# Kernel optimization log

Hardware: AMD Instinct MI355X
Metric: run time of the kernel (lower is better)

The kernel has to match this reference:

```python
import jax, jax.numpy as jnp
import numpy as np

C = 4096
C8 = C // 8  # 512, must equal h*w
B, H, W = 32, 16, 32


def setup_inputs() -> dict:
    key = jax.random.key(0)
    ks = jax.random.split(key, 8)
    s = 0.02
    return {
        "x": jax.random.normal(ks[0], (B, C, H, W), dtype=jnp.float32),
        "Wq": jax.random.normal(ks[1], (C8, C), dtype=jnp.float32) * s,
        "bq": jax.random.normal(ks[2], (C8,), dtype=jnp.float32) * s,
        "Wk": jax.random.normal(ks[3], (C8, C), dtype=jnp.float32) * s,
        "bk": jax.random.normal(ks[4], (C8,), dtype=jnp.float32) * s,
        "Wv": jax.random.normal(ks[5], (C, C), dtype=jnp.float32) * s,
        "bv": jax.random.normal(ks[6], (C,), dtype=jnp.float32) * s,
        "gamma": jax.random.normal(ks[7], (1,), dtype=jnp.float32),
    }


def reference(x, Wq, bq, Wk, bk, Wv, bv, gamma):
    b, c, h, w = x.shape
    xf = x.reshape(b, c, h * w)               # (b, c, hw)
    # 1x1 conv == per-position linear over channels
    q = jnp.einsum("oc,bcl->bol", Wq, xf) + bq[None, :, None]   # (b, c8, hw)
    k = jnp.einsum("oc,bcl->bol", Wk, xf) + bk[None, :, None]   # (b, c8, hw)
    v = jnp.einsum("oc,bcl->bol", Wv, xf) + bv[None, :, None]   # (b, c, hw)
    # energy = bmm(Q, K^T): (b, c8, c8); no sqrt(d) scaling (faithful)
    energy = jnp.einsum("bol,bpl->bop", q, k)
    attn = jax.nn.softmax(energy, axis=-1)
    # out = bmm(V, attn^T): out[b,c,p] = sum_k V[b,c,k] * attn[b,p,k]
    out = jnp.einsum("bck,bpk->bcp", v, attn)  # requires hw == c8
    out = out.reshape(b, c, h, w)
    return gamma * out + x
```

## Files before the change

### kernel.cpp

```cpp
#include <hip/hip_runtime.h>


typedef _Float16 f16;
typedef _Float16 h8 __attribute__((ext_vector_type(8)));
typedef _Float16 h4 __attribute__((ext_vector_type(4)));
typedef float fx4 __attribute__((ext_vector_type(4)));

#define CC  4096
#define C8  512
#define HWD 512
#define NB  32

__device__ __forceinline__ void stage_tile(const f16* __restrict__ g, f16* __restrict__ s, int ld) {
  const int t = threadIdx.x;
#pragma unroll
  for (int i = 0; i < 4; ++i) {
    const int id = t + i * 256;
    const int r = id >> 3, j = id & 7;
    const uint4 v = *reinterpret_cast<const uint4*>(g + (long)r * ld + (j << 3));
    char* p = reinterpret_cast<char*>(s);
    const int b = ((r << 7) + (j << 4)) ^ ((r & 7) << 4);
    *reinterpret_cast<uint4*>(p + b) = v;
  }
}

__device__ __forceinline__ h8 ldfrag(const f16* s, int row, int kb) {
  const int b = ((row << 7) + kb) ^ ((row & 7) << 4);
  return *reinterpret_cast<const h8*>(reinterpret_cast<const char*>(s) + b);
}

template<bool TRIPLE, int EPI>
__global__ __launch_bounds__(256) void gemm_ker(
    const f16* __restrict__ Ah, const f16* __restrict__ Al,
    const f16* __restrict__ Bh, const f16* __restrict__ Bl,
    int K, int lda, int ldb, long sAb, long sBb, long sCb, int ldc,
    const float* __restrict__ bias,
    float* __restrict__ Cf, f16* __restrict__ Ch, f16* __restrict__ Cl,
    const float* __restrict__ resid, const float* __restrict__ gam)
{
  constexpr int TILE = 128 * 64;
  __shared__ __align__(16) f16 smem[(TRIPLE ? 4 : 2) * TILE];
  f16* sAh = smem;
  f16* sBh = smem + TILE;
  f16* sAl = TRIPLE ? smem + 2 * TILE : nullptr;
  f16* sBl = TRIPLE ? smem + 3 * TILE : nullptr;

  const int bz = blockIdx.z;
  const int m0 = blockIdx.y * 128, n0 = blockIdx.x * 128;
  const f16* gA = Ah + (long)bz * sAb + (long)m0 * lda;
  const f16* gB = Bh + (long)bz * sBb + (long)n0 * ldb;

  const int lane = threadIdx.x & 63;
  const int wid  = threadIdx.x >> 6;
  const int wr = wid >> 1, wc = wid & 1;
  const int frow = lane & 15;
  const int kq = (lane >> 4) << 4;

  fx4 acc[4][4] = {};

  for (int k0 = 0; k0 < K; k0 += 64) {
    stage_tile(gA + k0, sAh, lda);
    stage_tile(gB + k0, sBh, ldb);
    if constexpr (TRIPLE) {
      stage_tile(Al + (long)bz * sAb + (long)m0 * lda + k0, sAl, lda);
      stage_tile(Bl + (long)bz * sBb + (long)n0 * ldb + k0, sBl, ldb);
    }
    __syncthreads();
#pragma unroll
    for (int ks = 0; ks < 2; ++ks) {
      const int kb = ks * 64 + kq;
      h8 aH[4], bH[4];
      h8 aL[4], bL[4];
#pragma unroll
      for (int f = 0; f < 4; ++f) {
        aH[f] = ldfrag(sAh, wr * 64 + f * 16 + frow, kb);
        bH[f] = ldfrag(sBh, wc * 64 + f * 16 + frow, kb);
        if constexpr (TRIPLE) {
          aL[f] = ldfrag(sAl, wr * 64 + f * 16 + frow, kb);
          bL[f] = ldfrag(sBl, wc * 64 + f * 16 + frow, kb);
        }
      }
#pragma unroll
      for (int fm = 0; fm < 4; ++fm)
#pragma unroll
        for (int fn = 0; fn < 4; ++fn) {
          acc[fm][fn] = __builtin_amdgcn_mfma_f32_16x16x32_f16(aH[fm], bH[fn], acc[fm][fn], 0, 0, 0);
          if constexpr (TRIPLE) {
            acc[fm][fn] = __builtin_amdgcn_mfma_f32_16x16x32_f16(aH[fm], bL[fn], acc[fm][fn], 0, 0, 0);
            acc[fm][fn] = __builtin_amdgcn_mfma_f32_16x16x32_f16(aL[fm], bH[fn], acc[fm][fn], 0, 0, 0);
          }
        }
    }
    __syncthreads();
  }

  const int cm = (lane >> 4) * 4;
  const int cn = lane & 15;
  const float g0 = (EPI == 3) ? gam[0] : 0.f;
#pragma unroll
  for (int fm = 0; fm < 4; ++fm) {
    const int gr0 = m0 + wr * 64 + fm * 16 + cm;
#pragma unroll
    for (int fn = 0; fn < 4; ++fn) {
      const int gc = n0 + wc * 64 + fn * 16 + cn;
#pragma unroll
      for (int j = 0; j < 4; ++j) {
        const int gr = gr0 + j;
        const long ci = (long)bz * sCb + (long)gr * ldc + gc;
        float v = acc[fm][fn][j];
        if constexpr (EPI == 0) {
          v += bias[gr];
          const f16 h = (f16)v;
          Ch[ci] = h;
          Cl[ci] = (f16)(v - (float)h);
        } else if constexpr (EPI == 1) {
          Ch[ci] = (f16)(v + bias[gr]);
        } else if constexpr (EPI == 2) {
          Cf[ci] = v;
        } else {
          Cf[ci] = g0 * v + resid[ci];
        }
      }
    }
  }
}

__global__ void transpose_split_k(const float* __restrict__ x, f16* __restrict__ xh, f16* __restrict__ xl) {
  __shared__ float t[32][33];
  const int l0 = blockIdx.x * 32, c0 = blockIdx.y * 32;
  const long bi = (long)blockIdx.z * CC * HWD;
  const long bo = (long)blockIdx.z * HWD * CC;
  const int tx = threadIdx.x, ty = threadIdx.y;
#pragma unroll
  for (int i = 0; i < 32; i += 8)
    t[ty + i][tx] = x[bi + (long)(c0 + ty + i) * HWD + l0 + tx];
  __syncthreads();
#pragma unroll
  for (int i = 0; i < 32; i += 8) {
    const float v = t[tx][ty + i];
    const f16 h = (f16)v;
    const long o = bo + (long)(l0 + ty + i) * CC + c0 + tx;
    xh[o] = h;
    xl[o] = (f16)(v - (float)h);
  }
}

template<bool HASLO>
__global__ void split_k(const float* __restrict__ in, f16* __restrict__ hi, f16* __restrict__ lo, long n) {
  const long i = ((long)blockIdx.x * blockDim.x + threadIdx.x) * 4;
  if (i >= n) return;
  const float4 v = *reinterpret_cast<const float4*>(in + i);
  const float vv[4] = {v.x, v.y, v.z, v.w};
  h4 h, l;
#pragma unroll
  for (int j = 0; j < 4; ++j) {
    const f16 hh = (f16)vv[j];
    h[j] = hh;
    l[j] = (f16)(vv[j] - (float)hh);
  }
  *reinterpret_cast<h4*>(hi + i) = h;
  if constexpr (HASLO) *reinterpret_cast<h4*>(lo + i) = l;
}

__global__ __launch_bounds__(256) void softmax_k(const float* __restrict__ E, f16* __restrict__ attn) {
  const int lane = threadIdx.x & 63;
  const int wid  = threadIdx.x >> 6;
  const long row = (long)blockIdx.x * 4 + wid;
  const float* e = E + row * 512;
  const float4 a = *reinterpret_cast<const float4*>(e + lane * 8);
  const float4 b = *reinterpret_cast<const float4*>(e + lane * 8 + 4);
  float vv[8] = {a.x, a.y, a.z, a.w, b.x, b.y, b.z, b.w};
  float m = vv[0];
#pragma unroll
  for (int i = 1; i < 8; ++i) m = fmaxf(m, vv[i]);
#pragma unroll
  for (int s = 32; s > 0; s >>= 1) m = fmaxf(m, __shfl_xor(m, s));
  float sum = 0.f;
  float ex[8];
#pragma unroll
  for (int i = 0; i < 8; ++i) { ex[i] = __expf(vv[i] - m); sum += ex[i]; }
#pragma unroll
  for (int s = 32; s > 0; s >>= 1) sum += __shfl_xor(sum, s);
  const float inv = 1.f / sum;
  h8 o;
#pragma unroll
  for (int i = 0; i < 8; ++i) o[i] = (f16)(ex[i] * inv);
  *reinterpret_cast<h8*>(attn + row * 512 + lane * 8) = o;
}

extern "C" void kernel_launch(void* const* d_in, const int* in_sizes, int n_in,
                              void* d_out, int out_size, void* d_ws, size_t ws_size,
                              hipStream_t stream) {
  const float* x  = (const float*)d_in[0];
  const float* Wq = (const float*)d_in[1];
  const float* bq = (const float*)d_in[2];
  const float* Wk = (const float*)d_in[3];
  const float* bk = (const float*)d_in[4];
  const float* Wv = (const float*)d_in[5];
  const float* bv = (const float*)d_in[6];
  const float* gm = (const float*)d_in[7];
  float* out = (float*)d_out;

  const size_t szXT = (size_t)NB * HWD * CC;
  const size_t szQK = (size_t)NB * C8 * HWD;
  const size_t szW  = (size_t)C8 * CC;
  const size_t szWv = (size_t)CC * CC;
  const size_t needBytes = (2 * szXT + 4 * szQK + 4 * szW + szWv) * sizeof(f16);
  if (ws_size < needBytes) return;

  f16* xT_h = (f16*)d_ws;
  f16* xT_l = xT_h + szXT;
  f16* v16  = xT_l;
  f16* q_h  = xT_h + 2 * szXT;
  f16* q_l  = q_h + szQK;
  f16* k_h  = q_l + szQK;
  f16* k_l  = k_h + szQK;
  f16* wq_h = k_l + szQK;
  f16* wq_l = wq_h + szW;
  f16* wk_h = wq_l + szW;
  f16* wk_l = wk_h + szW;
  f16* attn = wq_h;
  f16* wv_h = wk_l + szW;
  float* E  = (float*)wv_h;

  split_k<true ><<<dim3((C8 * CC) / 1024), 256, 0, stream>>>(Wq, wq_h, wq_l, (long)C8 * CC);
  split_k<true ><<<dim3((C8 * CC) / 1024), 256, 0, stream>>>(Wk, wk_h, wk_l, (long)C8 * CC);
  split_k<false><<<dim3((CC * CC) / 1024), 256, 0, stream>>>(Wv, wv_h, nullptr, (long)CC * CC);
  transpose_split_k<<<dim3(HWD / 32, CC / 32, NB), dim3(32, 8), 0, stream>>>(x, xT_h, xT_l);
  gemm_ker<true, 0><<<dim3(4, 4, NB), 256, 0, stream>>>(wq_h, wq_l, xT_h, xT_l, CC, CC, CC,
      0L, (long)HWD * CC, (long)C8 * HWD, HWD, bq, nullptr, q_h, q_l, nullptr, nullptr);
  gemm_ker<true, 0><<<dim3(4, 4, NB), 256, 0, stream>>>(wk_h, wk_l, xT_h, xT_l, CC, CC, CC,
      0L, (long)HWD * CC, (long)C8 * HWD, HWD, bk, nullptr, k_h, k_l, nullptr, nullptr);
  gemm_ker<false, 1><<<dim3(4, 32, NB), 256, 0, stream>>>(wv_h, nullptr, xT_h, nullptr, CC, CC, CC,
      0L, (long)HWD * CC, (long)CC * HWD, HWD, bv, nullptr, v16, nullptr, nullptr, nullptr);
  gemm_ker<true, 2><<<dim3(4, 4, NB), 256, 0, stream>>>(q_h, q_l, k_h, k_l, HWD, HWD, HWD,
      (long)C8 * HWD, (long)C8 * HWD, (long)C8 * C8, C8, nullptr, E, nullptr, nullptr, nullptr, nullptr);
  softmax_k<<<dim3(NB * C8 / 4), 256, 0, stream>>>(E, attn);
  gemm_ker<false, 3><<<dim3(4, 32, NB), 256, 0, stream>>>(v16, nullptr, attn, nullptr, HWD, HWD, HWD,
      (long)CC * HWD, (long)C8 * HWD, (long)CC * HWD, HWD, nullptr, out, nullptr, nullptr, x, gm);
}
```

Measured before the change: 1.468 ms.

## Add double-buffered 256x256 GEMM with direct global-to-LDS loads for V and output

Adds a new GEMM kernel that uses 256x256 output tiles with 512 threads and double-buffered LDS filled by global_load_lds. It interleaves fragment loads with MFMA issue and raises wave priority during MFMA runs. The kernel also remaps blocks so consecutive workgroups share operand tiles. It replaces the two big single-precision-f16 GEMMs (V projection and attn-V output) to cut per-tile load/sync stalls and raise reuse. The old kernel is trimmed to a triple-f16 variant for the Q/K GEMMs. The large LDS footprint (128KB) and hand-placed waitcnts risk occupancy limits and correctness if the counts are wrong.

```diff
diff --git a/kernel.cpp b/kernel.cpp
--- a/kernel.cpp
+++ b/kernel.cpp
@@ -10,6 +10,117 @@
 #define C8  512
 #define HWD 512
 #define NB  32
+
+
+__device__ __forceinline__ h8 ldfragC(const char* s, int row, int cb) {
+  const int b = ((row << 7) | cb) ^ ((row & 7) << 4);
+  return *reinterpret_cast<const h8*>(s + b);
+}
+
+#define AS1C(p) ((const __attribute__((address_space(1))) unsigned int*)(p))
+#define AS3(p)  ((__attribute__((address_space(3))) unsigned int*)(p))
+
+#define STAGE(bufsel) { \
+  char* la_ = smem + ((bufsel) << 16); \
+  char* lb_ = la_ + 32768; \
+  _Pragma("unroll") for (int q = 0; q < 4; ++q) { \
+    __builtin_amdgcn_global_load_lds(AS1C(pA[q]), AS3(la_ + (q << 13) + w1024), 16, 0, 0); \
+    __builtin_amdgcn_global_load_lds(AS1C(pB[q]), AS3(lb_ + (q << 13) + w1024), 16, 0, 0); \
+    pA[q] += 128; pB[q] += 128; } }
+
+#define LOADA(hm) { \
+  _Pragma("unroll") for (int f = 0; f < 4; ++f) \
+  _Pragma("unroll") for (int ks = 0; ks < 2; ++ks) \
+    a[f][ks] = ldfragC(At, wr * 128 + (hm) * 64 + f * 16 + frow, ks * 64 + kq); }
+
+#define LOADB(hn) { \
+  _Pragma("unroll") for (int g = 0; g < 2; ++g) \
+  _Pragma("unroll") for (int ks = 0; ks < 2; ++ks) \
+    b[g][ks] = ldfragC(Bt, wc * 64 + (hn) * 32 + g * 16 + frow, ks * 64 + kq); }
+
+#define MMA(hm, hn) { \
+  __builtin_amdgcn_s_setprio(1); \
+  _Pragma("unroll") for (int f = 0; f < 4; ++f) \
+  _Pragma("unroll") for (int g = 0; g < 2; ++g) \
+  _Pragma("unroll") for (int ks = 0; ks < 2; ++ks) \
+    acc[(hm) * 4 + f][(hn) * 2 + g] = __builtin_amdgcn_mfma_f32_16x16x32_f16( \
+        a[f][ks], b[g][ks], acc[(hm) * 4 + f][(hn) * 2 + g], 0, 0, 0); \
+  __builtin_amdgcn_s_setprio(0); }
+
+template<int EPI>
+__global__ __launch_bounds__(512, 2) void gemm256(
+    const f16* __restrict__ Ah, const f16* __restrict__ Bh,
+    int lda, int ldb, long sAb, long sBb, long sCb, int ldc, int K,
+    const float* __restrict__ bias, float* __restrict__ Cf, f16* __restrict__ Ch,
+    const float* __restrict__ resid, const float* __restrict__ gam)
+{
+  extern __shared__ __align__(16) char smem[];
+  const int F  = blockIdx.x;
+  const int Vv = ((F & 7) << 7) | (F >> 3);
+  const int bz = Vv >> 5;
+  const int m0 = (Vv & 15) << 8;
+  const int n0 = ((Vv >> 4) & 1) << 8;
+
+  const int T = threadIdx.x;
+  const int lane = T & 63;
+  const int w = T >> 6;
+  const int wr = w >> 2, wc = w & 3;
+  const int frow = lane & 15;
+  const int kq = (lane >> 4) << 4;
+  const int w1024 = w << 10;
+
+  const int rr = T >> 3;
+  const int corig = ((T & 7) << 4) ^ ((rr & 7) << 4);
+  const char* pA[4];
+  const char* pB[4];
+#pragma unroll
+  for (int q = 0; q < 4; ++q) {
+    pA[q] = (const char*)(Ah + bz * sAb + (long)(m0 + q * 64 + rr) * lda) + corig;
+    pB[q] = (const char*)(Bh + bz * sBb + (long)(n0 + q * 64 + rr) * ldb) + corig;
+  }
+
+  fx4 acc[8][4] = {};
+  const int nt = K >> 6;
+
+  STAGE(0)
+  for (int t = 0; t < nt; ++t) {
+    if (t + 1 < nt) {
+      STAGE((t + 1) & 1)
+      asm volatile("s_waitcnt vmcnt(8)" ::: "memory");
+    } else {
+      asm volatile("s_waitcnt vmcnt(0)" ::: "memory");
+    }
+    asm volatile("s_barrier" ::: "memory");
+    const char* At = smem + ((t & 1) << 16);
+    const char* Bt = At + 32768;
+    h8 a[4][2], b[2][2];
+    LOADA(0) LOADB(0) MMA(0, 0)
+    LOADA(1)          MMA(1, 0)
+              LOADB(1) MMA(1, 1)
+    LOADA(0)          MMA(0, 1)
+    __builtin_amdgcn_sched_barrier(0);
+    asm volatile("s_waitcnt lgkmcnt(0)" ::: "memory");
+    asm volatile("s_barrier" ::: "memory");
+  }
+
+  const int cm = (lane >> 4) << 2;
+  const int cn = lane & 15;
+  const float g0 = (EPI == 3) ? gam[0] : 0.f;
+#pragma unroll
+  for (int fm = 0; fm < 8; ++fm) {
+    const int gr0 = m0 + wr * 128 + fm * 16 + cm;
+#pragma unroll
+    for (int fn = 0; fn < 4; ++fn) {
+      const int gc = n0 + wc * 64 + fn * 16 + cn;
+#pragma unroll
+      for (int j = 0; j < 4; ++j) {
+        const long ci = bz * sCb + (long)(gr0 + j) * ldc + gc;
+        if constexpr (EPI == 1) Ch[ci] = (f16)(acc[fm][fn][j] + bias[gr0 + j]);
+        else                    Cf[ci] = g0 * acc[fm][fn][j] + resid[ci];
+      }
+    }
+  }
+}
 
 __device__ __forceinline__ void stage_tile(const f16* __restrict__ g, f16* __restrict__ s, int ld) {
   const int t = threadIdx.x;
@@ -29,21 +140,20 @@
   return *reinterpret_cast<const h8*>(reinterpret_cast<const char*>(s) + b);
 }
 
-template<bool TRIPLE, int EPI>
-__global__ __launch_bounds__(256) void gemm_ker(
+template<int EPI>
+__global__ __launch_bounds__(256) void gemm_tri(
     const f16* __restrict__ Ah, const f16* __restrict__ Al,
     const f16* __restrict__ Bh, const f16* __restrict__ Bl,
     int K, int lda, int ldb, long sAb, long sBb, long sCb, int ldc,
     const float* __restrict__ bias,
-    float* __restrict__ Cf, f16* __restrict__ Ch, f16* __restrict__ Cl,
-    const float* __restrict__ resid, const float* __restrict__ gam)
+    float* __restrict__ Cf, f16* __restrict__ Ch, f16* __restrict__ Cl)
 {
   constexpr int TILE = 128 * 64;
-  __shared__ __align__(16) f16 smem[(TRIPLE ? 4 : 2) * TILE];
+  __shared__ __align__(16) f16 smem[4 * TILE];
   f16* sAh = smem;
   f16* sBh = smem + TILE;
-  f16* sAl = TRIPLE ? smem + 2 * TILE : nullptr;
-  f16* sBl = TRIPLE ? smem + 3 * TILE : nullptr;
+  f16* sAl = smem + 2 * TILE;
+  f16* sBl = smem + 3 * TILE;
 
   const int bz = blockIdx.z;
   const int m0 = blockIdx.y * 128, n0 = blockIdx.x * 128;
@@ -61,34 +171,27 @@
   for (int k0 = 0; k0 < K; k0 += 64) {
     stage_tile(gA + k0, sAh, lda);
     stage_tile(gB + k0, sBh, ldb);
-    if constexpr (TRIPLE) {
-      stage_tile(Al + (long)bz * sAb + (long)m0 * lda + k0, sAl, lda);
-      stage_tile(Bl + (long)bz * sBb + (long)n0 * ldb + k0, sBl, ldb);
-    }
+    stage_tile(Al + (long)bz * sAb + (long)m0 * lda + k0, sAl, lda);
+    stage_tile(Bl + (long)bz * sBb + (long)n0 * ldb + k0, sBl, ldb);
     __syncthreads();
 #pragma unroll
     for (int ks = 0; ks < 2; ++ks) {
       const int kb = ks * 64 + kq;
-      h8 aH[4], bH[4];
-      h8 aL[4], bL[4];
+      h8 aH[4], bH[4], aL[4], bL[4];
 #pragma unroll
       for (int f = 0; f < 4; ++f) {
         aH[f] = ldfrag(sAh, wr * 64 + f * 16 + frow, kb);
         bH[f] = ldfrag(sBh, wc * 64 + f * 16 + frow, kb);
-        if constexpr (TRIPLE) {
-          aL[f] = ldfrag(sAl, wr * 64 + f * 16 + frow, kb);
-          bL[f] = ldfrag(sBl, wc * 64 + f * 16 + frow, kb);
-        }
+        aL[f] = ldfrag(sAl, wr * 64 + f * 16 + frow, kb);
+        bL[f] = ldfrag(sBl, wc * 64 + f * 16 + frow, kb);
       }
 #pragma unroll
       for (int fm = 0; fm < 4; ++fm)
 #pragma unroll
         for (int fn = 0; fn < 4; ++fn) {
           acc[fm][fn] = __builtin_amdgcn_mfma_f32_16x16x32_f16(aH[fm], bH[fn], acc[fm][fn], 0, 0, 0);
-          if constexpr (TRIPLE) {
-            acc[fm][fn] = __builtin_amdgcn_mfma_f32_16x16x32_f16(aH[fm], bL[fn], acc[fm][fn], 0, 0, 0);
-            acc[fm][fn] = __builtin_amdgcn_mfma_f32_16x16x32_f16(aL[fm], bH[fn], acc[fm][fn], 0, 0, 0);
-          }
+          acc[fm][fn] = __builtin_amdgcn_mfma_f32_16x16x32_f16(aH[fm], bL[fn], acc[fm][fn], 0, 0, 0);
+          acc[fm][fn] = __builtin_amdgcn_mfma_f32_16x16x32_f16(aL[fm], bH[fn], acc[fm][fn], 0, 0, 0);
         }
     }
     __syncthreads();
@@ -96,7 +199,6 @@
 
   const int cm = (lane >> 4) * 4;
   const int cn = lane & 15;
-  const float g0 = (EPI == 3) ? gam[0] : 0.f;
 #pragma unroll
   for (int fm = 0; fm < 4; ++fm) {
     const int gr0 = m0 + wr * 64 + fm * 16 + cm;
@@ -113,12 +215,8 @@
           const f16 h = (f16)v;
           Ch[ci] = h;
           Cl[ci] = (f16)(v - (float)h);
-        } else if constexpr (EPI == 1) {
-          Ch[ci] = (f16)(v + bias[gr]);
-        } else if constexpr (EPI == 2) {
+        } else {
           Cf[ci] = v;
-        } else {
-          Cf[ci] = g0 * v + resid[ci];
         }
       }
     }
@@ -227,15 +325,15 @@
   split_k<true ><<<dim3((C8 * CC) / 1024), 256, 0, stream>>>(Wk, wk_h, wk_l, (long)C8 * CC);
   split_k<false><<<dim3((CC * CC) / 1024), 256, 0, stream>>>(Wv, wv_h, nullptr, (long)CC * CC);
   transpose_split_k<<<dim3(HWD / 32, CC / 32, NB), dim3(32, 8), 0, stream>>>(x, xT_h, xT_l);
-  gemm_ker<true, 0><<<dim3(4, 4, NB), 256, 0, stream>>>(wq_h, wq_l, xT_h, xT_l, CC, CC, CC,
-      0L, (long)HWD * CC, (long)C8 * HWD, HWD, bq, nullptr, q_h, q_l, nullptr, nullptr);
-  gemm_ker<true, 0><<<dim3(4, 4, NB), 256, 0, stream>>>(wk_h, wk_l, xT_h, xT_l, CC, CC, CC,
-      0L, (long)HWD * CC, (long)C8 * HWD, HWD, bk, nullptr, k_h, k_l, nullptr, nullptr);
-  gemm_ker<false, 1><<<dim3(4, 32, NB), 256, 0, stream>>>(wv_h, nullptr, xT_h, nullptr, CC, CC, CC,
-      0L, (long)HWD * CC, (long)CC * HWD, HWD, bv, nullptr, v16, nullptr, nullptr, nullptr);
-  gemm_ker<true, 2><<<dim3(4, 4, NB), 256, 0, stream>>>(q_h, q_l, k_h, k_l, HWD, HWD, HWD,
-      (long)C8 * HWD, (long)C8 * HWD, (long)C8 * C8, C8, nullptr, E, nullptr, nullptr, nullptr, nullptr);
+  gemm_tri<0><<<dim3(4, 4, NB), 256, 0, stream>>>(wq_h, wq_l, xT_h, xT_l, CC, CC, CC,
+      0L, (long)HWD * CC, (long)C8 * HWD, HWD, bq, nullptr, q_h, q_l);
+  gemm_tri<0><<<dim3(4, 4, NB), 256, 0, stream>>>(wk_h, wk_l, xT_h, xT_l, CC, CC, CC,
+      0L, (long)HWD * CC, (long)C8 * HWD, HWD, bk, nullptr, k_h, k_l);
+  gemm256<1><<<dim3(1024), 512, 131072, stream>>>(wv_h, xT_h, CC, CC,
+      0L, (long)HWD * CC, (long)CC * HWD, HWD, CC, bv, nullptr, v16, nullptr, nullptr);
+  gemm_tri<2><<<dim3(4, 4, NB), 256, 0, stream>>>(q_h, q_l, k_h, k_l, HWD, HWD, HWD,
+      (long)C8 * HWD, (long)C8 * HWD, (long)C8 * C8, C8, nullptr, E, nullptr, nullptr);
   softmax_k<<<dim3(NB * C8 / 4), 256, 0, stream>>>(E, attn);
-  gemm_ker<false, 3><<<dim3(4, 32, NB), 256, 0, stream>>>(v16, nullptr, attn, nullptr, HWD, HWD, HWD,
-      (long)CC * HWD, (long)C8 * HWD, (long)CC * HWD, HWD, nullptr, out, nullptr, nullptr, x, gm);
-}
+  gemm256<3><<<dim3(1024), 512, 131072, stream>>>(v16, attn, HWD, HWD,
+      (long)CC * HWD, (long)C8 * HWD, (long)CC * HWD, HWD, C8, nullptr, out, nullptr, x, gm);
+}
```

New measurement: 1.369 ms. -6.7%, faster.
